# Performance work log

Measured on AMD Instinct MI355X. Metric: run time of the kernel, lower is better.

Reference implementation:

```python
import jax, jax.numpy as jnp
import numpy as np

_J6 = jnp.array([[0,0,0,0,0,1],[0,0,0,0,-1,0],[0,0,0,1,0,0],
                 [0,0,1,0,0,0],[0,-1,0,0,0,0],[1,0,0,0,0,0]], dtype=jnp.float32)
_PAIRS4 = [(0,1),(0,2),(0,3),(1,2),(1,3),(2,3)]
H = 16  # n_heads

def _ln(x, g, b, eps=1e-5):
    m = jnp.mean(x, axis=-1, keepdims=True)
    v = jnp.var(x, axis=-1, keepdims=True)
    return (x - m) / jnp.sqrt(v + eps) * g + b

def _exterior(p1, p2):
    # Plucker coordinates of the line through p1,p2 in R^4 -> R^6, normalized
    parts = [p1[..., i] * p2[..., j] - p1[..., j] * p2[..., i] for i, j in _PAIRS4]
    L = jnp.stack(parts, axis=-1)
    n = jnp.linalg.norm(L, axis=-1, keepdims=True)
    return L / jnp.maximum(n, 1e-12)

def _iterated_gram_attn(x, Wqkv, bqkv, W1w, W2w, W1r, W2r, Wmv, bmv, Wmg, bmg,
                        mem_scale, iter_mix, decay_logits, Wout, bout):
    B, T, D = x.shape
    dh = D // H
    # ---- standard causal attention branch ----
    qkv = (x @ Wqkv + bqkv).reshape(B, T, 3, H, dh)
    q = jnp.transpose(qkv[:, :, 0], (0, 2, 1, 3))  # bhtd
    k = jnp.transpose(qkv[:, :, 1], (0, 2, 1, 3))
    v = jnp.transpose(qkv[:, :, 2], (0, 2, 1, 3))
    scores = jnp.einsum('bhtd,bhsd->bhts', q, k) * (dh ** -0.5)
    causal = jnp.tril(jnp.ones((T, T), dtype=bool))
    scores = jnp.where(causal, scores, -jnp.inf)
    attn = jax.nn.softmax(scores, axis=-1)  # dropout is eval-mode identity
    seq_out = jnp.einsum('bhts,bhsd->bhtd', attn, v).transpose(0, 2, 1, 3).reshape(B, T, D)
    # ---- Gram memory branch ----
    x_prev = jnp.concatenate([jnp.zeros_like(x[:, :1]), x[:, :-1]], axis=1)
    w1 = (x_prev @ W1w).reshape(B, T, H, 4)
    w2 = (x @ W2w).reshape(B, T, H, 4)
    write_lines = _exterior(w1, w2)                       # (B,T,H,6)
    r1 = (x @ W1r).reshape(B, T, H, 4)
    r2 = (x @ W2r).reshape(B, T, H, 4)
    read_lines = _exterior(r1, r2)                        # (B,T,H,6)
    Jw = jnp.einsum('bthi,ij->bhtj', write_lines, _J6)    # (B,H,T,6)
    rd = jnp.transpose(read_lines, (0, 2, 1, 3))          # (B,H,T,6)
    decays = jax.nn.sigmoid(decay_logits)                 # (H,)
    pos = jnp.arange(T, dtype=x.dtype)
    outer = Jw[..., :, None] * Jw[..., None, :]           # (B,H,T,6,6)
    dinv = (1.0 / jnp.maximum(decays, 1e-6))[:, None] ** pos[None, :]  # (H,T)
    M = jnp.cumsum(outer * dinv[None, :, :, None, None], axis=2)
    M = jnp.concatenate([jnp.zeros_like(M[:, :, :1]), M[:, :, :-1]], axis=2)  # shift: strictly past
    dfwd = decays[:, None] ** pos[None, :]
    M = M * dfwd[None, :, :, None, None]                  # (B,H,T,6,6)
    rdM = jnp.einsum('bhti,bhtij->bhtj', rd, M)
    score_M = jnp.sum(rdM * rd, axis=-1)                  # (B,H,T)
    score_M2 = jnp.sum(rdM * rdM, axis=-1)
    alpha = jax.nn.sigmoid(iter_mix[0])
    mem_score = (1 - alpha) * score_M + alpha * score_M2
    mem_val = x @ Wmv + bmv                               # (B,T,D)
    gate = jax.nn.sigmoid(x @ Wmg + bmg)                  # (B,T,H)
    gated = jax.nn.sigmoid(jnp.transpose(mem_score, (0, 2, 1)) * mem_scale[None, None, :]) * gate
    gated = jnp.mean(gated, axis=-1, keepdims=True)       # (B,T,1)
    return (seq_out + gated * mem_val) @ Wout + bout

def _block(x, ln1_g, ln1_b, Wqkv, bqkv, W1w, W2w, W1r, W2r, Wmv, bmv, Wmg, bmg,
           mem_scale, iter_mix, decay_logits, Wout, bout,
           ln2_g, ln2_b, Wfc, bfc, Wproj, bproj):
    h = _ln(x, ln1_g, ln1_b)
    x = x + _iterated_gram_attn(h, Wqkv, bqkv, W1w, W2w, W1r, W2r, Wmv, bmv,
                                Wmg, bmg, mem_scale, iter_mix, decay_logits, Wout, bout)
    h2 = _ln(x, ln2_g, ln2_b)
    mlp = jax.nn.gelu(h2 @ Wfc + bfc, approximate=False) @ Wproj + bproj
    return x + mlp

def setup_inputs() -> dict:
    key = jax.random.key(0)
    B, T, D = 2, 1024, 1024
    dff = 4 * D
    ks = jax.random.split(key, 16)
    s = 0.02
    inp = {
        'x': jax.random.normal(ks[0], (B, T, D), jnp.float32),
        'ln1_g': jnp.ones((D,), jnp.float32), 'ln1_b': jnp.zeros((D,), jnp.float32),
        'Wqkv': jax.random.normal(ks[1], (D, 3 * D), jnp.float32) * s,
        'bqkv': jnp.zeros((3 * D,), jnp.float32),
        'W1w': jax.random.normal(ks[2], (D, 4 * H), jnp.float32) * s,
        'W2w': jax.random.normal(ks[3], (D, 4 * H), jnp.float32) * s,
        'W1r': jax.random.normal(ks[4], (D, 4 * H), jnp.float32) * s,
        'W2r': jax.random.normal(ks[5], (D, 4 * H), jnp.float32) * s,
        'Wmv': jax.random.normal(ks[6], (D, D), jnp.float32) * s,
        'bmv': jnp.zeros((D,), jnp.float32),
        'Wmg': jax.random.normal(ks[7], (D, H), jnp.float32) * s,
        'bmg': jnp.zeros((H,), jnp.float32),
        'mem_scale': jnp.full((H,), 0.1, jnp.float32),
        'iter_mix': jnp.zeros((1,), jnp.float32),
        'decay_logits': jnp.full((H,), 4.6, jnp.float32) + 0.1 * jax.random.normal(ks[8], (H,), jnp.float32),
        'Wout': jax.random.normal(ks[9], (D, D), jnp.float32) * s,
        'bout': jnp.zeros((D,), jnp.float32),
        'ln2_g': jnp.ones((D,), jnp.float32), 'ln2_b': jnp.zeros((D,), jnp.float32),
        'Wfc': jax.random.normal(ks[10], (D, dff), jnp.float32) * s,
        'bfc': jnp.zeros((dff,), jnp.float32),
        'Wproj': jax.random.normal(ks[11], (dff, D), jnp.float32) * s,
        'bproj': jnp.zeros((D,), jnp.float32),
    }
    return inp

def reference(x, ln1_g, ln1_b, Wqkv, bqkv, W1w, W2w, W1r, W2r, Wmv, bmv, Wmg, bmg,
              mem_scale, iter_mix, decay_logits, Wout, bout,
              ln2_g, ln2_b, Wfc, bfc, Wproj, bproj):
    return _block(x, ln1_g, ln1_b, Wqkv, bqkv, W1w, W2w, W1r, W2r, Wmv, bmv, Wmg, bmg,
                  mem_scale, iter_mix, decay_logits, Wout, bout,
                  ln2_g, ln2_b, Wfc, bfc, Wproj, bproj)
```

## Files before the change

### kernel.cpp

```cpp
#include <hip/hip_runtime.h>
#include <hip/hip_bf16.h>
#include <math.h>

typedef float f32x4 __attribute__((ext_vector_type(4)));
typedef _Float16 f16x8 __attribute__((ext_vector_type(8)));
typedef _Float16 f16x4 __attribute__((ext_vector_type(4)));

#define TT 1024
#define DD 1024
#define QS 4608

typedef __attribute__((address_space(1))) const void gas_void;
typedef __attribute__((address_space(3))) void las_void;
static __device__ __forceinline__ void gl_lds16(const void* g, void* l) {
  __builtin_amdgcn_global_load_lds((gas_void*)g, (las_void*)l, 16, 0, 0);
}

__global__ __launch_bounds__(256) void gemm_t16(
    const _Float16* __restrict__ A, const _Float16* __restrict__ Wt,
    const float* __restrict__ bias, void* __restrict__ Cv,
    int N, int K, int act, int gx, int mode, int ktiles) {
  __shared__ __align__(16) _Float16 As[128 * 32];
  __shared__ __align__(16) _Float16 Bs[128 * 32];
  const int tid = threadIdx.x;
  const int lane = tid & 63;
  const int wid = tid >> 6;
  const int wr = wid >> 1, wc = wid & 1;
  const int g = lane >> 4, l16 = lane & 15;
  const int cpx = gridDim.x >> 3;
  const int wg = (blockIdx.x & 7) * cpx + (blockIdx.x >> 3);
  const int row0 = (wg / gx) * 128, col0 = (wg % gx) * 128;
  const int kbeg = blockIdx.y * ktiles * 32;

  f32x4 acc[4][4];
#pragma unroll
  for (int m = 0; m < 4; ++m)
#pragma unroll
    for (int n = 0; n < 4; ++n) acc[m][n] = (f32x4){0.f, 0.f, 0.f, 0.f};

  const int prm = (l16 >> 1) & 3;

  for (int kt = 0; kt < ktiles; ++kt) {
    if (kt) __syncthreads();
    const int kp = kbeg + kt * 32;
#pragma unroll
    for (int i = 0; i < 2; ++i) {
      const int rr = i * 64 + (tid >> 2);
      const int qq = (tid & 3) ^ ((rr >> 1) & 3);
      gl_lds16(A + (size_t)(row0 + rr) * K + kp + (qq << 3),
               (char*)As + (i * 256 + wid * 64) * 16);
      gl_lds16(Wt + (size_t)(col0 + rr) * K + kp + (qq << 3),
               (char*)Bs + (i * 256 + wid * 64) * 16);
    }
    __syncthreads();
    f16x8 af[4], bf[4];
#pragma unroll
    for (int m = 0; m < 4; ++m) {
      const int r = wr * 64 + m * 16 + l16;
      af[m] = *(const f16x8*)(As + r * 32 + ((g ^ prm) << 3));
    }
#pragma unroll
    for (int n = 0; n < 4; ++n) {
      const int r = wc * 64 + n * 16 + l16;
      bf[n] = *(const f16x8*)(Bs + r * 32 + ((g ^ prm) << 3));
    }
#pragma unroll
    for (int m = 0; m < 4; ++m)
#pragma unroll
      for (int n = 0; n < 4; ++n)
        acc[m][n] = __builtin_amdgcn_mfma_f32_16x16x32_f16(af[m], bf[n], acc[m][n], 0, 0, 0);
  }
#pragma unroll
  for (int m = 0; m < 4; ++m) {
#pragma unroll
    for (int n = 0; n < 4; ++n) {
      const int col = col0 + wc * 64 + n * 16 + l16;
      const float bv = (mode != 2 && bias) ? bias[col] : 0.f;
#pragma unroll
      for (int rg = 0; rg < 4; ++rg) {
        const int row = row0 + wr * 64 + m * 16 + g * 4 + rg;
        const size_t off = (size_t)row * N + col;
        float v = acc[m][n][rg] + bv;
        if (act == 1) v = 0.5f * v * (1.f + erff(v * 0.70710678118654752f));
        if (mode == 2) atomicAdd(&((float*)Cv)[off], v);
        else ((_Float16*)Cv)[off] = (_Float16)v;
      }
    }
  }
}

__global__ __launch_bounds__(256) void transT(const float* __restrict__ W,
                                              _Float16* __restrict__ WT, int K, int N) {
  __shared__ float tile[64][65];
  const int n0 = blockIdx.x * 64, k0 = blockIdx.y * 64;
  const int tn = threadIdx.x & 63, tk4 = threadIdx.x >> 6;
#pragma unroll
  for (int it = 0; it < 16; ++it) {
    const int k = k0 + it * 4 + tk4;
    tile[tn][it * 4 + tk4] = W[(size_t)k * N + n0 + tn];
  }
  __syncthreads();
  const int on = threadIdx.x >> 2, ok = threadIdx.x & 3;
  f16x8 a, b;
#pragma unroll
  for (int j = 0; j < 8; ++j) {
    a[j] = (_Float16)tile[on][ok * 16 + j];
    b[j] = (_Float16)tile[on][ok * 16 + 8 + j];
  }
  _Float16* dst = WT + (size_t)(n0 + on) * K + k0 + ok * 16;
  *(f16x8*)dst = a;
  *(f16x8*)(dst + 8) = b;
}

__global__ __launch_bounds__(256) void prep_megaT(
    const float* __restrict__ Wqkv, const float* __restrict__ W1w, const float* __restrict__ W2w,
    const float* __restrict__ W1r, const float* __restrict__ W2r, const float* __restrict__ Wmg,
    const float* __restrict__ Wmv, _Float16* __restrict__ WmT) {
  __shared__ float tile[64][65];
  const int n0 = blockIdx.x * 64, k0 = blockIdx.y * 64;
  const int tn = threadIdx.x & 63, tk4 = threadIdx.x >> 6;
#pragma unroll
  for (int it = 0; it < 16; ++it) {
    const int k = k0 + it * 4 + tk4;
    const int n = n0 + tn;
    float v;
    if (n < 3072) v = Wqkv[(size_t)k * 3072 + n];
    else if (n < 3136) v = W1w[k * 64 + n - 3072];
    else if (n < 3200) v = W2w[k * 64 + n - 3136];
    else if (n < 3264) v = W1r[k * 64 + n - 3200];
    else if (n < 3328) v = W2r[k * 64 + n - 3264];
    else if (n < 3344) v = Wmg[k * 16 + n - 3328];
    else if (n < 3584) v = 0.f;
    else v = Wmv[(size_t)k * 1024 + n - 3584];
    tile[tn][it * 4 + tk4] = v;
  }
  __syncthreads();
  const int on = threadIdx.x >> 2, ok = threadIdx.x & 3;
  f16x8 a, b;
#pragma unroll
  for (int j = 0; j < 8; ++j) {
    a[j] = (_Float16)tile[on][ok * 16 + j];
    b[j] = (_Float16)tile[on][ok * 16 + 8 + j];
  }
  _Float16* dst = WmT + (size_t)(n0 + on) * 1024 + k0 + ok * 16;
  *(f16x8*)dst = a;
  *(f16x8*)(dst + 8) = b;
}

__global__ void bm_init(const float* __restrict__ bqkv, const float* __restrict__ bmg,
                        const float* __restrict__ bmv, float* __restrict__ bm) {
  const int col = blockIdx.x * 256 + threadIdx.x;
  if (col >= 4608) return;
  float b = 0.f;
  if (col < 3072) b = bqkv[col];
  else if (col >= 3328 && col < 3344) b = bmg[col - 3328];
  else if (col >= 3584) b = bmv[col - 3584];
  bm[col] = b;
}

__global__ __launch_bounds__(256) void ln16(const float* __restrict__ in,
    const float* __restrict__ gw, const float* __restrict__ bw, _Float16* __restrict__ out) {
  const int row = blockIdx.x, tid = threadIdx.x;
  const float* x = in + (size_t)row * DD;
  const float4 v = *(const float4*)(x + tid * 4);
  float s = v.x + v.y + v.z + v.w;
  float sq = v.x * v.x + v.y * v.y + v.z * v.z + v.w * v.w;
#pragma unroll
  for (int off = 32; off >= 1; off >>= 1) { s += __shfl_xor(s, off); sq += __shfl_xor(sq, off); }
  __shared__ float red[8];
  const int lane = tid & 63, wv = tid >> 6;
  if (lane == 0) { red[wv] = s; red[4 + wv] = sq; }
  __syncthreads();
  s = red[0] + red[1] + red[2] + red[3];
  sq = red[4] + red[5] + red[6] + red[7];
  const float mean = s * (1.f / 1024.f);
  const float var = sq * (1.f / 1024.f) - mean * mean;
  const float rstd = rsqrtf(var + 1e-5f);
  const float4 g4 = *(const float4*)(gw + tid * 4);
  const float4 b4 = *(const float4*)(bw + tid * 4);
  f16x4 o;
  o[0] = (_Float16)((v.x - mean) * rstd * g4.x + b4.x);
  o[1] = (_Float16)((v.y - mean) * rstd * g4.y + b4.y);
  o[2] = (_Float16)((v.z - mean) * rstd * g4.z + b4.z);
  o[3] = (_Float16)((v.w - mean) * rstd * g4.w + b4.w);
  *(f16x4*)(out + (size_t)row * DD + tid * 4) = o;
}

static __device__ __forceinline__ int swzA(int row, int k) {
  return row * 64 + ((((k >> 3) ^ row) & 7) << 3) + (k & 7);
}
static __device__ __forceinline__ int swzV(int row, int k) {
  return row * 64 + ((((k >> 3) ^ row ^ (row >> 3)) & 7) << 3) + (k & 7);
}

__global__ __launch_bounds__(256) void attn_mfma(const _Float16* __restrict__ qkv,
                                                 _Float16* __restrict__ seq_out) {
  __shared__ __align__(16) _Float16 Kl[64 * 64];
  __shared__ __align__(16) _Float16 Vt[64 * 64];
  __shared__ __align__(16) _Float16 Pl[4][16 * 64];
  const int tid = threadIdx.x, lane = tid & 63, wq = tid >> 6;
  const int g = lane >> 4, l16 = lane & 15;
  const int qt = blockIdx.x, hh = blockIdx.y, bb = blockIdx.z;
  const int nt = qt + 1;

  f16x8 qf[2];
  {
    const _Float16* qp = qkv + (size_t)(bb * TT + qt * 64 + wq * 16 + l16) * QS + hh * 64;
#pragma unroll
    for (int ks = 0; ks < 2; ++ks) {
      const f16x8 a = *(const f16x8*)(qp + ks * 32 + g * 8);
#pragma unroll
      for (int j = 0; j < 8; ++j) qf[ks][j] = (_Float16)((float)a[j] * 0.125f);
    }
  }

  f32x4 oacc[4];
#pragma unroll
  for (int n = 0; n < 4; ++n) oacc[n] = (f32x4){0.f, 0.f, 0.f, 0.f};
  float m[4] = {-INFINITY, -INFINITY, -INFINITY, -INFINITY};
  float l[4] = {0.f, 0.f, 0.f, 0.f};

  const int skey = tid >> 2, sc4 = tid & 3;

  for (int tt = 0; tt < nt; ++tt) {
    if (tt) __syncthreads();
    {
      const _Float16* kp = qkv + (size_t)(bb * TT + tt * 64 + skey) * QS + hh * 64 + 1024;
      const _Float16* vp = kp + 1024;
#pragma unroll
      for (int ii = 0; ii < 4; ++ii) {
        const int d0 = sc4 * 4 + ii * 16;
        *(f16x4*)(Kl + swzA(skey, d0)) = *(const f16x4*)(kp + d0);
        const f16x4 vv = *(const f16x4*)(vp + d0);
        Vt[swzV(d0 + 0, skey)] = vv[0];
        Vt[swzV(d0 + 1, skey)] = vv[1];
        Vt[swzV(d0 + 2, skey)] = vv[2];
        Vt[swzV(d0 + 3, skey)] = vv[3];
      }
    }
    __syncthreads();
    f32x4 s[4];
#pragma unroll
    for (int n = 0; n < 4; ++n) s[n] = (f32x4){0.f, 0.f, 0.f, 0.f};
#pragma unroll
    for (int ks = 0; ks < 2; ++ks) {
      f16x8 kf[4];
#pragma unroll
      for (int n = 0; n < 4; ++n) kf[n] = *(const f16x8*)(Kl + swzA(n * 16 + l16, ks * 32 + g * 8));
#pragma unroll
      for (int n = 0; n < 4; ++n)
        s[n] = __builtin_amdgcn_mfma_f32_16x16x32_f16(qf[ks], kf[n], s[n], 0, 0, 0);
    }
    if (tt == qt) {
      const int rloc = wq * 16 + g * 4;
#pragma unroll
      for (int n = 0; n < 4; ++n) {
        const int cloc = n * 16 + l16;
#pragma unroll
        for (int reg = 0; reg < 4; ++reg)
          if (cloc > rloc + reg) s[n][reg] = -INFINITY;
      }
    }
    float f[4];
#pragma unroll
    for (int reg = 0; reg < 4; ++reg) {
      float t = fmaxf(fmaxf(s[0][reg], s[1][reg]), fmaxf(s[2][reg], s[3][reg]));
#pragma unroll
      for (int off = 1; off < 16; off <<= 1) t = fmaxf(t, __shfl_xor(t, off));
      const float nm = fmaxf(m[reg], t);
      f[reg] = __expf(m[reg] - nm);
      m[reg] = nm;
    }
    float rs[4] = {0.f, 0.f, 0.f, 0.f};
#pragma unroll
    for (int n = 0; n < 4; ++n) {
#pragma unroll
      for (int reg = 0; reg < 4; ++reg) {
        const float p = __expf(s[n][reg] - m[reg]);
        rs[reg] += p;
        Pl[wq][swzA(g * 4 + reg, n * 16 + l16)] = (_Float16)p;
      }
    }
#pragma unroll
    for (int reg = 0; reg < 4; ++reg) {
      float t = rs[reg];
#pragma unroll
      for (int off = 1; off < 16; off <<= 1) t += __shfl_xor(t, off);
      l[reg] = l[reg] * f[reg] + t;
    }
#pragma unroll
    for (int n = 0; n < 4; ++n)
#pragma unroll
      for (int reg = 0; reg < 4; ++reg) oacc[n][reg] *= f[reg];
#pragma unroll
    for (int ks = 0; ks < 2; ++ks) {
      const f16x8 pa = *(const f16x8*)(Pl[wq] + swzA(l16, ks * 32 + g * 8));
      f16x8 vb[4];
#pragma unroll
      for (int n = 0; n < 4; ++n) vb[n] = *(const f16x8*)(Vt + swzV(n * 16 + l16, ks * 32 + g * 8));
#pragma unroll
      for (int n = 0; n < 4; ++n)
        oacc[n] = __builtin_amdgcn_mfma_f32_16x16x32_f16(pa, vb[n], oacc[n], 0, 0, 0);
    }
  }
#pragma unroll
  for (int n = 0; n < 4; ++n) {
#pragma unroll
    for (int reg = 0; reg < 4; ++reg) {
      const int r = qt * 64 + wq * 16 + g * 4 + reg;
      seq_out[(size_t)(bb * TT + r) * DD + hh * 64 + n * 16 + l16] = (_Float16)(oacc[n][reg] / l[reg]);
    }
  }
}

static __device__ __forceinline__ void ext6(const float* a, const float* b, float* L) {
  L[0] = a[0] * b[1] - a[1] * b[0];
  L[1] = a[0] * b[2] - a[2] * b[0];
  L[2] = a[0] * b[3] - a[3] * b[0];
  L[3] = a[1] * b[2] - a[2] * b[1];
  L[4] = a[1] * b[3] - a[3] * b[1];
  L[5] = a[2] * b[3] - a[3] * b[2];
  const float n = sqrtf(L[0]*L[0] + L[1]*L[1] + L[2]*L[2] + L[3]*L[3] + L[4]*L[4] + L[5]*L[5]);
  const float s = 1.f / fmaxf(n, 1e-12f);
#pragma unroll
  for (int i = 0; i < 6; ++i) L[i] *= s;
}

__global__ void lines_post(const _Float16* __restrict__ mega, float* __restrict__ jw,
                           float* __restrict__ rdv, float* __restrict__ gate) {
  const int idx = blockIdx.x * 256 + threadIdx.x;
  const int h = idx & 15;
  const int bt = idx >> 4;
  const int t = bt & 1023;
  const int b = bt >> 10;
  const _Float16* row = mega + (size_t)bt * QS + 3072;
  float w1[4] = {0.f, 0.f, 0.f, 0.f}, w2[4], r1[4], r2[4];
  if (t > 0) {
#pragma unroll
    for (int i = 0; i < 4; ++i) w1[i] = (float)row[-QS + h * 4 + i];
  }
#pragma unroll
  for (int i = 0; i < 4; ++i) {
    w2[i] = (float)row[64 + h * 4 + i];
    r1[i] = (float)row[128 + h * 4 + i];
    r2[i] = (float)row[192 + h * 4 + i];
  }
  const float gp = (float)row[256 + h];
  float wl[6], rl[6];
  ext6(w1, w2, wl);
  ext6(r1, r2, rl);
  const size_t o = ((size_t)(b * 16 + h) * 1024 + t) * 6;
  jw[o + 0] =  wl[5]; jw[o + 1] = -wl[4]; jw[o + 2] =  wl[3];
  jw[o + 3] =  wl[2]; jw[o + 4] = -wl[1]; jw[o + 5] =  wl[0];
#pragma unroll
  for (int i = 0; i < 6; ++i) rdv[o + i] = rl[i];
  gate[idx] = 1.f / (1.f + __expf(-gp));
}

static __device__ __forceinline__ int midx(int i, int j) {
  return (i <= j) ? (i * (13 - i)) / 2 + (j - i) : (j * (13 - j)) / 2 + (i - j);
}

__global__ __launch_bounds__(64) void gram_scan(const float* __restrict__ jwv,
    const float* __restrict__ rdv, const float* __restrict__ decay_logits,
    const float* __restrict__ iter_mix, float* __restrict__ mem_score) {
  const int h = blockIdx.x & 15, b = blockIdx.x >> 4;
  const int lane = threadIdx.x;
  const float decay = 1.f / (1.f + __expf(-decay_logits[h]));
  const float alpha = 1.f / (1.f + __expf(-iter_mix[0]));
  __shared__ float sd[64 * 193];
  const size_t base = (size_t)(b * 16 + h) * 1024 * 6;
  for (int it = 0; it < 96; ++it) {
    const int idx = it * 64 + lane;
    const int t = idx / 6, i = idx - 6 * t;
    const int ld = t >> 4, s = t & 15;
    sd[ld * 193 + s * 6 + i] = jwv[base + idx];
    sd[ld * 193 + 96 + s * 6 + i] = rdv[base + idx];
  }
  __syncthreads();
  const float* seg = sd + lane * 193;

  float C[21];
#pragma unroll
  for (int e = 0; e < 21; ++e) C[e] = 0.f;
  for (int s = 0; s < 16; ++s) {
    float J[6], dJ[6];
#pragma unroll
    for (int i = 0; i < 6; ++i) { J[i] = seg[s * 6 + i]; dJ[i] = decay * J[i]; }
#pragma unroll
    for (int i = 0; i < 6; ++i)
#pragma unroll
      for (int j = i; j < 6; ++j)
        C[midx(i, j)] = decay * C[midx(i, j)] + dJ[i] * J[j];
  }
  const float d2 = decay * decay, d4 = d2 * d2, d8 = d4 * d4;
  float fk = d8 * d8;
#pragma unroll
  for (int k = 0; k < 6; ++k) {
    const int off = 1 << k;
#pragma unroll
    for (int e = 0; e < 21; ++e) {
      const float u = __shfl(C[e], lane - off);
      if (lane >= off) C[e] += fk * u;
    }
    fk = fk * fk;
  }
  float M[21];
#pragma unroll
  for (int e = 0; e < 21; ++e) {
    const float u = __shfl(C[e], lane - 1);
    M[e] = (lane >= 1) ? u : 0.f;
  }
  float* msp = mem_score + (size_t)(b * 16 + h) * 1024 + lane * 16;
  for (int s = 0; s < 16; ++s) {
    float J[6], r[6];
#pragma unroll
    for (int i = 0; i < 6; ++i) { J[i] = seg[s * 6 + i]; r[i] = seg[96 + s * 6 + i]; }
    float rdM[6];
#pragma unroll
    for (int i = 0; i < 6; ++i) {
      float a = 0.f;
#pragma unroll
      for (int j = 0; j < 6; ++j) a += M[midx(i, j)] * r[j];
      rdM[i] = a;
    }
    float s1 = 0.f, s2 = 0.f;
#pragma unroll
    for (int i = 0; i < 6; ++i) { s1 += rdM[i] * r[i]; s2 += rdM[i] * rdM[i]; }
    msp[s] = (1.f - alpha) * s1 + alpha * s2;
    float dJ[6];
#pragma unroll
    for (int i = 0; i < 6; ++i) dJ[i] = decay * J[i];
#pragma unroll
    for (int i = 0; i < 6; ++i)
#pragma unroll
      for (int j = i; j < 6; ++j)
        M[midx(i, j)] = decay * M[midx(i, j)] + dJ[i] * J[j];
  }
}

__global__ void gmean_kernel(const float* __restrict__ ms, const float* __restrict__ gate,
    const float* __restrict__ mem_scale, float* __restrict__ gm) {
  const int bt = blockIdx.x * 256 + threadIdx.x;
  const int b = bt >> 10, t = bt & 1023;
  float acc = 0.f;
#pragma unroll
  for (int h = 0; h < 16; ++h) {
    const float sc = ms[(size_t)(b * 16 + h) * 1024 + t];
    const float gt = gate[(size_t)bt * 16 + h];
    acc += (1.f / (1.f + __expf(-sc * mem_scale[h]))) * gt;
  }
  gm[bt] = acc * (1.f / 16.f);
}

__global__ void combine_kernel(const _Float16* __restrict__ seq, const _Float16* __restrict__ mega,
    const float* __restrict__ gm, _Float16* __restrict__ outp) {
  const int i = blockIdx.x * 256 + threadIdx.x;
  const int bt = i >> 8, c4 = i & 255;
  const float g = gm[bt];
  const f16x4 s4 = *(const f16x4*)(seq + (size_t)i * 4);
  const f16x4 m4 = *(const f16x4*)(mega + (size_t)bt * QS + 3584 + c4 * 4);
  f16x4 o;
#pragma unroll
  for (int j = 0; j < 4; ++j) o[j] = (_Float16)((float)s4[j] + g * (float)m4[j]);
  *(f16x4*)(outp + (size_t)i * 4) = o;
}

__global__ void addb_init(const float* __restrict__ src, const float* __restrict__ bias,
                          float* __restrict__ dst) {
  const size_t i = (size_t)blockIdx.x * 256 + threadIdx.x;
  const int c4 = (int)(i & 255);
  const float4 s = ((const float4*)src)[i];
  const float4 b = ((const float4*)bias)[c4];
  float4 o;
  o.x = s.x + b.x; o.y = s.y + b.y; o.z = s.z + b.z; o.w = s.w + b.w;
  ((float4*)dst)[i] = o;
}

extern "C" void kernel_launch(void* const* d_in, const int* in_sizes, int n_in,
                              void* d_out, int out_size, void* d_ws, size_t ws_size,
                              hipStream_t stream) {
  (void)in_sizes; (void)n_in; (void)out_size; (void)ws_size;
  const float* x       = (const float*)d_in[0];
  const float* ln1_g   = (const float*)d_in[1];
  const float* ln1_b   = (const float*)d_in[2];
  const float* Wqkv    = (const float*)d_in[3];
  const float* bqkv    = (const float*)d_in[4];
  const float* W1w     = (const float*)d_in[5];
  const float* W2w     = (const float*)d_in[6];
  const float* W1r     = (const float*)d_in[7];
  const float* W2r     = (const float*)d_in[8];
  const float* Wmv     = (const float*)d_in[9];
  const float* bmv     = (const float*)d_in[10];
  const float* Wmg     = (const float*)d_in[11];
  const float* bmg     = (const float*)d_in[12];
  const float* mscale  = (const float*)d_in[13];
  const float* itermix = (const float*)d_in[14];
  const float* dlogits = (const float*)d_in[15];
  const float* Wout    = (const float*)d_in[16];
  const float* bout    = (const float*)d_in[17];
  const float* ln2_g   = (const float*)d_in[18];
  const float* ln2_b   = (const float*)d_in[19];
  const float* Wfc     = (const float*)d_in[20];
  const float* bfc     = (const float*)d_in[21];
  const float* Wproj   = (const float*)d_in[22];
  const float* bproj   = (const float*)d_in[23];
  float* out = (float*)d_out;
  float* ws = (float*)d_ws;

  const size_t M1 = 1u << 20;
  _Float16* h16    = (_Float16*)ws;
  _Float16* WmT    = (_Float16*)(ws + 1 * M1);
  float*    bm     = ws + 3407872;
  float*    jw     = ws + 3538944;
  float*    rd     = ws + 3538944 + 196608;
  float*    gate   = ws + 3538944 + 393216;
  float*    ms     = ws + 3538944 + 425984;
  float*    gm     = ws + 3538944 + 458752;
  float*    y      = ws + 4 * M1;
  _Float16* mega   = (_Float16*)(ws + 6 * M1);
  _Float16* fc16   = (_Float16*)(ws + 6 * M1);
  _Float16* seq16  = (_Float16*)(ws + 11010048);
  _Float16* WoutT  = (_Float16*)(ws + 12058624);
  _Float16* WfcT   = (_Float16*)(ws + 12 * M1);
  _Float16* WprojT = (_Float16*)(ws + 14 * M1);

  prep_megaT<<<dim3(72, 16), 256, 0, stream>>>(Wqkv, W1w, W2w, W1r, W2r, Wmg, Wmv, WmT);
  bm_init<<<18, 256, 0, stream>>>(bqkv, bmg, bmv, bm);
  transT<<<dim3(16, 16), 256, 0, stream>>>(Wout, WoutT, 1024, 1024);
  transT<<<dim3(64, 16), 256, 0, stream>>>(Wfc, WfcT, 1024, 4096);
  transT<<<dim3(16, 64), 256, 0, stream>>>(Wproj, WprojT, 4096, 1024);

  ln16<<<2048, 256, 0, stream>>>(x, ln1_g, ln1_b, h16);
  gemm_t16<<<576, 256, 0, stream>>>(h16, WmT, bm, mega, 4608, 1024, 0, 36, 1, 32);
  attn_mfma<<<dim3(16, 16, 2), 256, 0, stream>>>(mega, seq16);
  lines_post<<<128, 256, 0, stream>>>(mega, jw, rd, gate);
  gram_scan<<<32, 64, 0, stream>>>(jw, rd, dlogits, itermix, ms);
  gmean_kernel<<<8, 256, 0, stream>>>(ms, gate, mscale, gm);
  combine_kernel<<<2048, 256, 0, stream>>>(seq16, mega, gm, h16);
  addb_init<<<2048, 256, 0, stream>>>(x, bout, y);
  gemm_t16<<<dim3(128, 4), 256, 0, stream>>>(h16, WoutT, nullptr, y, 1024, 1024, 0, 8, 2, 8);
  ln16<<<2048, 256, 0, stream>>>(y, ln2_g, ln2_b, h16);
  gemm_t16<<<512, 256, 0, stream>>>(h16, WfcT, bfc, fc16, 4096, 1024, 1, 32, 1, 32);
  addb_init<<<2048, 256, 0, stream>>>(y, bproj, out);
  gemm_t16<<<dim3(128, 4), 256, 0, stream>>>(fc16, WprojT, nullptr, out, 1024, 4096, 0, 8, 2, 32);
}
```

Before: 258.7 us.

## Triple-buffer GEMM LDS loads with 512-thread blocks and fuse gate-mean into combine

The GEMM kernel moves to 512 threads (8 waves, each covering a 32x64 sub-tile) and a three-stage LDS ring. Tile loads are issued two k-steps ahead, with vmcnt waits and one barrier per iteration, so global-to-LDS transfers overlap the MFMA work and the per-tile double barrier goes away. Separately, the gate-mean kernel is folded into the combine kernel, with one block per token computing its 16-head term in shared memory, which drops a launch and the gm buffer. LDS use triples and per-wave register tiles shrink, which may change occupancy and arithmetic intensity per wave.

```diff
diff --git a/kernel.cpp b/kernel.cpp
--- a/kernel.cpp
+++ b/kernel.cpp
@@ -16,12 +16,12 @@
   __builtin_amdgcn_global_load_lds((gas_void*)g, (las_void*)l, 16, 0, 0);
 }
 
-__global__ __launch_bounds__(256) void gemm_t16(
+__global__ __launch_bounds__(512) void gemm_t16(
     const _Float16* __restrict__ A, const _Float16* __restrict__ Wt,
     const float* __restrict__ bias, void* __restrict__ Cv,
     int N, int K, int act, int gx, int mode, int ktiles) {
-  __shared__ __align__(16) _Float16 As[128 * 32];
-  __shared__ __align__(16) _Float16 Bs[128 * 32];
+  __shared__ __align__(16) _Float16 As[3][128 * 32];
+  __shared__ __align__(16) _Float16 Bs[3][128 * 32];
   const int tid = threadIdx.x;
   const int lane = tid & 63;
   const int wid = tid >> 6;
@@ -32,53 +32,66 @@
   const int row0 = (wg / gx) * 128, col0 = (wg % gx) * 128;
   const int kbeg = blockIdx.y * ktiles * 32;
 
-  f32x4 acc[4][4];
-#pragma unroll
-  for (int m = 0; m < 4; ++m)
+  f32x4 acc[2][4];
+#pragma unroll
+  for (int m = 0; m < 2; ++m)
 #pragma unroll
     for (int n = 0; n < 4; ++n) acc[m][n] = (f32x4){0.f, 0.f, 0.f, 0.f};
 
+  const int srow = tid >> 2;
+  const int goff = ((tid & 3) ^ ((srow >> 1) & 3)) << 3;
+  const _Float16* agp = A + (size_t)(row0 + srow) * K + kbeg + goff;
+  const _Float16* bgp = Wt + (size_t)(col0 + srow) * K + kbeg + goff;
+  const int ldst = tid * 16;
+
   const int prm = (l16 >> 1) & 3;
 
+  gl_lds16(agp, (char*)As[0] + ldst);
+  gl_lds16(bgp, (char*)Bs[0] + ldst);
+  if (1 < ktiles) {
+    gl_lds16(agp + 32, (char*)As[1] + ldst);
+    gl_lds16(bgp + 32, (char*)Bs[1] + ldst);
+  }
+
+  int cs = 0, ss = 2;
   for (int kt = 0; kt < ktiles; ++kt) {
-    if (kt) __syncthreads();
-    const int kp = kbeg + kt * 32;
-#pragma unroll
-    for (int i = 0; i < 2; ++i) {
-      const int rr = i * 64 + (tid >> 2);
-      const int qq = (tid & 3) ^ ((rr >> 1) & 3);
-      gl_lds16(A + (size_t)(row0 + rr) * K + kp + (qq << 3),
-               (char*)As + (i * 256 + wid * 64) * 16);
-      gl_lds16(Wt + (size_t)(col0 + rr) * K + kp + (qq << 3),
-               (char*)Bs + (i * 256 + wid * 64) * 16);
-    }
-    __syncthreads();
-    f16x8 af[4], bf[4];
-#pragma unroll
-    for (int m = 0; m < 4; ++m) {
-      const int r = wr * 64 + m * 16 + l16;
-      af[m] = *(const f16x8*)(As + r * 32 + ((g ^ prm) << 3));
+    if (kt < ktiles - 1) asm volatile("s_waitcnt vmcnt(2)" ::: "memory");
+    else                 asm volatile("s_waitcnt vmcnt(0)" ::: "memory");
+    __builtin_amdgcn_s_barrier();
+    __builtin_amdgcn_sched_barrier(0);
+    if (kt + 2 < ktiles) {
+      const int kp = (kt + 2) * 32;
+      gl_lds16(agp + kp, (char*)As[ss] + ldst);
+      gl_lds16(bgp + kp, (char*)Bs[ss] + ldst);
+    }
+    f16x8 af[2], bf[4];
+#pragma unroll
+    for (int m = 0; m < 2; ++m) {
+      const int r = wr * 32 + m * 16 + l16;
+      af[m] = *(const f16x8*)(As[cs] + r * 32 + ((g ^ prm) << 3));
     }
 #pragma unroll
     for (int n = 0; n < 4; ++n) {
       const int r = wc * 64 + n * 16 + l16;
-      bf[n] = *(const f16x8*)(Bs + r * 32 + ((g ^ prm) << 3));
-    }
-#pragma unroll
-    for (int m = 0; m < 4; ++m)
+      bf[n] = *(const f16x8*)(Bs[cs] + r * 32 + ((g ^ prm) << 3));
+    }
+#pragma unroll
+    for (int m = 0; m < 2; ++m)
 #pragma unroll
       for (int n = 0; n < 4; ++n)
         acc[m][n] = __builtin_amdgcn_mfma_f32_16x16x32_f16(af[m], bf[n], acc[m][n], 0, 0, 0);
-  }
-#pragma unroll
-  for (int m = 0; m < 4; ++m) {
+    cs = (cs == 2) ? 0 : cs + 1;
+    ss = (ss == 2) ? 0 : ss + 1;
+  }
+#pragma unroll
+  for (int m = 0; m < 2; ++m) {
 #pragma unroll
     for (int n = 0; n < 4; ++n) {
       const int col = col0 + wc * 64 + n * 16 + l16;
       const float bv = (mode != 2 && bias) ? bias[col] : 0.f;
 #pragma unroll
       for (int rg = 0; rg < 4; ++rg) {
-        const int row = row0 + wr * 64 + m * 16 + g * 4 + rg;
+        const int row = row0 + wr * 32 + m * 16 + g * 4 + rg;
         const size_t off = (size_t)row * N + col;
         float v = acc[m][n][rg] + bv;
         if (act == 1) v = 0.5f * v * (1.f + erff(v * 0.70710678118654752f));
@@ -439,31 +452,30 @@
   }
 }
 
-__global__ void gmean_kernel(const float* __restrict__ ms, const float* __restrict__ gate,
-    const float* __restrict__ mem_scale, float* __restrict__ gm) {
-  const int bt = blockIdx.x * 256 + threadIdx.x;
+__global__ __launch_bounds__(256) void combine_kernel(const _Float16* __restrict__ seq,
+    const _Float16* __restrict__ mega, const float* __restrict__ ms,
+    const float* __restrict__ gate, const float* __restrict__ mem_scale,
+    _Float16* __restrict__ outp) {
+  const int bt = blockIdx.x;
   const int b = bt >> 10, t = bt & 1023;
+  __shared__ float hterm[16];
+  const int tid = threadIdx.x;
+  if (tid < 16) {
+    const float sc = ms[(size_t)(b * 16 + tid) * 1024 + t];
+    const float gt = gate[(size_t)bt * 16 + tid];
+    hterm[tid] = (1.f / (1.f + __expf(-sc * mem_scale[tid]))) * gt;
+  }
+  __syncthreads();
   float acc = 0.f;
 #pragma unroll
-  for (int h = 0; h < 16; ++h) {
-    const float sc = ms[(size_t)(b * 16 + h) * 1024 + t];
-    const float gt = gate[(size_t)bt * 16 + h];
-    acc += (1.f / (1.f + __expf(-sc * mem_scale[h]))) * gt;
-  }
-  gm[bt] = acc * (1.f / 16.f);
-}
-
-__global__ void combine_kernel(const _Float16* __restrict__ seq, const _Float16* __restrict__ mega,
-    const float* __restrict__ gm, _Float16* __restrict__ outp) {
-  const int i = blockIdx.x * 256 + threadIdx.x;
-  const int bt = i >> 8, c4 = i & 255;
-  const float g = gm[bt];
-  const f16x4 s4 = *(const f16x4*)(seq + (size_t)i * 4);
-  const f16x4 m4 = *(const f16x4*)(mega + (size_t)bt * QS + 3584 + c4 * 4);
+  for (int h = 0; h < 16; ++h) acc += hterm[h];
+  const float g = acc * (1.f / 16.f);
+  const f16x4 s4 = *(const f16x4*)(seq + (size_t)bt * 1024 + tid * 4);
+  const f16x4 m4 = *(const f16x4*)(mega + (size_t)bt * QS + 3584 + tid * 4);
   f16x4 o;
 #pragma unroll
   for (int j = 0; j < 4; ++j) o[j] = (_Float16)((float)s4[j] + g * (float)m4[j]);
-  *(f16x4*)(outp + (size_t)i * 4) = o;
+  *(f16x4*)(outp + (size_t)bt * 1024 + tid * 4) = o;
 }
 
 __global__ void addb_init(const float* __restrict__ src, const float* __restrict__ bias,
@@ -516,7 +528,6 @@
   float*    rd     = ws + 3538944 + 196608;
   float*    gate   = ws + 3538944 + 393216;
   float*    ms     = ws + 3538944 + 425984;
-  float*    gm     = ws + 3538944 + 458752;
   float*    y      = ws + 4 * M1;
   _Float16* mega   = (_Float16*)(ws + 6 * M1);
   _Float16* fc16   = (_Float16*)(ws + 6 * M1);
@@ -532,16 +543,15 @@
   transT<<<dim3(16, 64), 256, 0, stream>>>(Wproj, WprojT, 4096, 1024);
 
   ln16<<<2048, 256, 0, stream>>>(x, ln1_g, ln1_b, h16);
-  gemm_t16<<<576, 256, 0, stream>>>(h16, WmT, bm, mega, 4608, 1024, 0, 36, 1, 32);
+  gemm_t16<<<576, 512, 0, stream>>>(h16, WmT, bm, mega, 4608, 1024, 0, 36, 1, 32);
   attn_mfma<<<dim3(16, 16, 2), 256, 0, stream>>>(mega, seq16);
   lines_post<<<128, 256, 0, stream>>>(mega, jw, rd, gate);
   gram_scan<<<32, 64, 0, stream>>>(jw, rd, dlogits, itermix, ms);
-  gmean_kernel<<<8, 256, 0, stream>>>(ms, gate, mscale, gm);
-  combine_kernel<<<2048, 256, 0, stream>>>(seq16, mega, gm, h16);
+  combine_kernel<<<2048, 256, 0, stream>>>(seq16, mega, ms, gate, mscale, h16);
   addb_init<<<2048, 256, 0, stream>>>(x, bout, y);
-  gemm_t16<<<dim3(128, 4), 256, 0, stream>>>(h16, WoutT, nullptr, y, 1024, 1024, 0, 8, 2, 8);
+  gemm_t16<<<dim3(128, 4), 512, 0, stream>>>(h16, WoutT, nullptr, y, 1024, 1024, 0, 8, 2, 8);
   ln16<<<2048, 256, 0, stream>>>(y, ln2_g, ln2_b, h16);
-  gemm_t16<<<512, 256, 0, stream>>>(h16, WfcT, bfc, fc16, 4096, 1024, 1, 32, 1, 32);
+  gemm_t16<<<512, 512, 0, stream>>>(h16, WfcT, bfc, fc16, 4096, 1024, 1, 32, 1, 32);
   addb_init<<<2048, 256, 0, stream>>>(y, bproj, out);
-  gemm_t16<<<dim3(128, 4), 256, 0, stream>>>(fc16, WprojT, nullptr, out, 1024, 4096, 0, 8, 2, 32);
-}
+  gemm_t16<<<dim3(128, 4), 512, 0, stream>>>(fc16, WprojT, nullptr, out, 1024, 4096, 0, 8, 2, 32);
+}
```

New measurement: 251.0 us. -3.0%, faster.
